# Performance work log

Measured on AMD Instinct MI355X. Metric: run time of the kernel, lower is better.

The kernel has to match this reference:

```python
import jax, jax.numpy as jnp
import numpy as np

EMBED_DIM = 256
NUM_HEADS = 8
HEAD_DIM = EMBED_DIM // NUM_HEADS
SCALE = HEAD_DIM ** -0.5  # note: scale uses head_dim even though attention is over full D
EPS = 1e-12  # torch F.normalize eps


def setup_inputs() -> dict:
    key = jax.random.key(0)
    k1, k2, k3 = jax.random.split(key, 3)
    B, Nq, Nk, D = 4, 4096, 4096, EMBED_DIM
    return {
        "query": jax.random.normal(k1, (B, Nq, D), dtype=jnp.float32),
        "key": jax.random.normal(k2, (B, Nk, D), dtype=jnp.float32),
        "value": jax.random.normal(k3, (B, Nk, D), dtype=jnp.float32),
    }


def _l2_normalize(x):
    # matches torch.nn.functional.normalize(x, dim=-1): x / max(||x||, eps)
    n = jnp.linalg.norm(x, axis=-1, keepdims=True)
    return x / jnp.maximum(n, EPS)


def reference(query, key, value):
    q = _l2_normalize(query)          # (B, Nq, D)
    k = _l2_normalize(key)            # (B, Nk, D)
    scores = jnp.einsum("bqd,bkd->bqk", q, k) * SCALE  # (B, Nq, Nk) cosine sims
    attn = jax.nn.softmax(scores, axis=-1)
    return jnp.einsum("bqk,bkd->bqd", attn, value)     # (B, Nq, D)
```

## Files before the change

### kernel.cpp

```cpp
#include <hip/hip_runtime.h>


#define NQ 4096
#define DIM 256
#define NROWS 16384
#define BM 64
#define BN 64
#define PSTRIDE 68

typedef __attribute__((ext_vector_type(8))) short bf16x8;
typedef __attribute__((ext_vector_type(4))) float f32x4;
typedef __attribute__((ext_vector_type(16))) float f32x16;

__device__ __forceinline__ unsigned short f2bf(float f) {
  unsigned int u = __float_as_uint(f);
  u += 0x7fffu + ((u >> 16) & 1u);
  return (unsigned short)(u >> 16);
}

__device__ __forceinline__ float bf2f(unsigned short h) {
  return __uint_as_float((unsigned int)h << 16);
}

__device__ __forceinline__ unsigned int pack2bf(float a, float b) {
  unsigned int ua = __float_as_uint(a) + 0x8000u;
  unsigned int ub = __float_as_uint(b) + 0x8000u;
  return __builtin_amdgcn_perm(ub, ua, 0x07060302u);
}

__device__ __forceinline__ void gload16(const void* g, void* l) {
  __builtin_amdgcn_global_load_lds(
      (const __attribute__((address_space(1))) unsigned int*)g,
      (__attribute__((address_space(3))) unsigned int*)l, 16, 0, 0);
}

__global__ __launch_bounds__(256) void prep(
    const float* __restrict__ K, const float* __restrict__ V,
    unsigned short* __restrict__ Kfm, unsigned short* __restrict__ Vfm)
{
  __shared__ unsigned short vt[32 * 264];
  const int blk = blockIdx.x, tid = threadIdx.x;
  const int wave = tid >> 6, lane = tid & 63;
  if (blk < 512) {
    const int kt2 = blk;
    const int kt = kt2 >> 1, h = kt2 & 1;
    #pragma unroll
    for (int i = 0; i < 8; i++) {
      const int r = wave*8 + i;
      float4 v = *(const float4*)(K + ((size_t)kt2*32 + r) * DIM + lane * 4);
      float ss = v.x*v.x + v.y*v.y + v.z*v.z + v.w*v.w;
      #pragma unroll
      for (int off = 1; off < 64; off <<= 1) ss += __shfl_xor(ss, off, 64);
      float scale = 1.0f / fmaxf(sqrtf(ss), 1e-12f);
      ushort4 o;
      o.x = f2bf(v.x*scale); o.y = f2bf(v.y*scale);
      o.z = f2bf(v.z*scale); o.w = f2bf(v.w*scale);
      *(ushort4*)(vt + r*264 + lane*4) = o;
    }
    __syncthreads();
    #pragma unroll
    for (int s = 0; s < 4; s++) {
      const int ch = tid + 256*s;
      const int c = ch >> 5, r = ch & 31;
      const int n = h*32 + r;
      bf16x8 val = *(const bf16x8*)(vt + r*264 + c*8);
      *(bf16x8*)(Kfm + (size_t)kt*16384 + (size_t)(c*64 + n)*8) = val;
    }
  } else {
    const int NS = blk - 512;
    #pragma unroll
    for (int i = 0; i < 4; i++) {
      const int e = tid + 256*i;
      const int nl = e >> 6, d = (e & 63) * 4;
      float4 v = *(const float4*)(V + ((size_t)NS*16 + nl)*DIM + d);
      ushort4 o;
      o.x = f2bf(v.x); o.y = f2bf(v.y); o.z = f2bf(v.z); o.w = f2bf(v.w);
      *(ushort4*)(vt + nl*264 + d) = o;
    }
    __syncthreads();
    #pragma unroll
    for (int i = 0; i < 2; i++) {
      const int ch = tid + 256*i;
      const int db = ch >> 6, ln = ch & 63;
      const int row0 = (ln >> 5) * 8, dd = db*32 + (ln & 31);
      ushort4 a, b;
      a.x = vt[(row0+0)*264 + dd]; a.y = vt[(row0+1)*264 + dd];
      a.z = vt[(row0+2)*264 + dd]; a.w = vt[(row0+3)*264 + dd];
      b.x = vt[(row0+4)*264 + dd]; b.y = vt[(row0+5)*264 + dd];
      b.z = vt[(row0+6)*264 + dd]; b.w = vt[(row0+7)*264 + dd];
      size_t base = ((size_t)(NS*8 + db)*64 + ln)*8;
      *(ushort4*)(Vfm + base)     = a;
      *(ushort4*)(Vfm + base + 4) = b;
    }
  }
}

template<int KS>
__global__ __launch_bounds__(256, 3) void attn(
    const float* __restrict__ Qg,
    const unsigned short* __restrict__ Kfm,
    const unsigned short* __restrict__ Vfm,
    unsigned short* __restrict__ Opart, float* __restrict__ lpart)
{
  constexpr int NITER = (NQ / KS) / BN;
  __shared__ unsigned short Klds[32 * 64 * 8];
  __shared__ unsigned short Plds[BM * PSTRIDE];

  const int tid = threadIdx.x, wave = tid >> 6, lane = tid & 63;
  const int l15 = lane & 15, l4 = lane >> 4;
  const int blk = blockIdx.x;
  const int g = blk & (4*KS - 1), qt = blk / (4*KS);
  const int b = g / KS, ks = g & (KS - 1);
  const int Rq0 = b*NQ + qt*BM;
  const int n0base = b*NQ + ks*(NQ/KS);
  const int mi = wave & 1, ni = wave >> 1;

  {
    unsigned short* Qlds = Klds;
    #pragma unroll
    for (int i = 0; i < 16; i++) {
      const int r = wave*16 + i;
      float4 v = *(const float4*)(Qg + (size_t)(Rq0 + r)*DIM + lane*4);
      float ss = v.x*v.x + v.y*v.y + v.z*v.z + v.w*v.w;
      #pragma unroll
      for (int off = 1; off < 64; off <<= 1) ss += __shfl_xor(ss, off, 64);
      float scale = (0.17677669529663687f * 1.4426950408889634f)
                    / fmaxf(sqrtf(ss), 1e-12f);
      ushort4 o;
      o.x = f2bf(v.x*scale); o.y = f2bf(v.y*scale);
      o.z = f2bf(v.z*scale); o.w = f2bf(v.w*scale);
      *(ushort4*)(Qlds + r*DIM + lane*4) = o;
    }
  }
  __syncthreads();

  bf16x8 qf[2][8];
  #pragma unroll
  for (int mt = 0; mt < 2; mt++) {
    const unsigned short* qrow = Klds + (mi*32 + mt*16 + l15)*DIM + l4*8;
    #pragma unroll
    for (int kg = 0; kg < 8; kg++)
      qf[mt][kg] = *(const bf16x8*)(qrow + kg*32);
  }
  __syncthreads();

  f32x16 oacc[2][2] = {};
  float lacc[2] = {};

  auto stage = [&](int kt_) {
    const unsigned short* src = Kfm + (size_t)((n0base + kt_*BN) >> 6) * (32*64*8);
    #pragma unroll
    for (int jj = 0; jj < 4; jj++) {
      const int c = wave*8 + jj*2;
      gload16(src + (size_t)c*512 + lane*8,     Klds + (size_t)c*512);
      gload16(src + (size_t)(c+1)*512 + lane*8, Klds + (size_t)(c+1)*512);
    }
  };

  stage(0);

  for (int kt = 0; kt < NITER; kt++) {
    __syncthreads();

    f32x4 sacc[2][2] = {};
    #pragma unroll
    for (int nt = 0; nt < 2; nt++) {
      const int nrow = ni*32 + nt*16 + l15;
      #pragma unroll
      for (int kg = 0; kg < 8; kg++) {
        const int c = kg*4 + l4;
        bf16x8 kf = *(const bf16x8*)(Klds + ((size_t)(c*64 + nrow))*8);
        __builtin_amdgcn_s_setprio(1);
        #pragma unroll
        for (int mt = 0; mt < 2; mt++)
          sacc[nt][mt] = __builtin_amdgcn_mfma_f32_16x16x32_bf16(
              kf, qf[mt][kg], sacc[nt][mt], 0, 0, 0);
        __builtin_amdgcn_s_setprio(0);
      }
    }

    #pragma unroll
    for (int nt = 0; nt < 2; nt++)
      #pragma unroll
      for (int mt = 0; mt < 2; mt++) {
        float p0 = __builtin_amdgcn_exp2f(sacc[nt][mt][0]);
        float p1 = __builtin_amdgcn_exp2f(sacc[nt][mt][1]);
        float p2 = __builtin_amdgcn_exp2f(sacc[nt][mt][2]);
        float p3 = __builtin_amdgcn_exp2f(sacc[nt][mt][3]);
        lacc[mt] += (p0 + p1) + (p2 + p3);
        uint2 pk;
        pk.x = pack2bf(p0, p1);
        pk.y = pack2bf(p2, p3);
        const int m = mi*32 + mt*16 + l15;
        const int n = ni*32 + nt*16 + 4*l4;
        *(uint2*)(Plds + m*PSTRIDE + n) = pk;
      }

    __syncthreads();

    if (kt + 1 < NITER) stage(kt + 1);

    const int NB0 = (n0base + kt*BN) >> 4;
    #pragma unroll
    for (int kstep = 0; kstep < 4; kstep++) {
      bf16x8 pf[2], vf[2];
      #pragma unroll
      for (int mt2 = 0; mt2 < 2; mt2++)
        pf[mt2] = *(const bf16x8*)(Plds + (mt2*32 + (lane & 31))*PSTRIDE
                                   + kstep*16 + 8*(lane >> 5));
      #pragma unroll
      for (int dt = 0; dt < 2; dt++) {
        const int db = wave*2 + dt;
        vf[dt] = *(const bf16x8*)(Vfm + ((size_t)((NB0 + kstep)*8 + db)*64 + lane)*8);
      }
      __builtin_amdgcn_s_setprio(1);
      #pragma unroll
      for (int mt2 = 0; mt2 < 2; mt2++)
        #pragma unroll
        for (int dt = 0; dt < 2; dt++)
          oacc[mt2][dt] = __builtin_amdgcn_mfma_f32_32x32x16_bf16(
              pf[mt2], vf[dt], oacc[mt2][dt], 0, 0, 0);
      __builtin_amdgcn_s_setprio(0);
    }
  }

  #pragma unroll
  for (int mt = 0; mt < 2; mt++) {
    float s = lacc[mt];
    s += __shfl_xor(s, 16, 64);
    s += __shfl_xor(s, 32, 64);
    if (l4 == 0)
      lpart[(size_t)(ks*2 + ni)*NROWS + Rq0 + mi*32 + mt*16 + l15] = s;
  }

  #pragma unroll
  for (int mt2 = 0; mt2 < 2; mt2++)
    #pragma unroll
    for (int dt = 0; dt < 2; dt++)
      #pragma unroll
      for (int reg = 0; reg < 16; reg++) {
        const int m = mt2*32 + 4*(lane >> 5) + (reg & 3) + 8*(reg >> 2);
        const int d = wave*64 + dt*32 + (lane & 31);
        Opart[((size_t)(ks*NROWS + Rq0 + m))*DIM + d] = f2bf(oacc[mt2][dt][reg]);
      }
}

template<int KS>
__global__ __launch_bounds__(256) void combine(
    const unsigned short* __restrict__ Opart, const float* __restrict__ lpart,
    float* __restrict__ out)
{
  const size_t idx = (size_t)blockIdx.x*256 + threadIdx.x;
  const size_t e = idx*4;
  const int R = (int)(e >> 8);
  float ls = 0.0f;
  #pragma unroll
  for (int i = 0; i < 2*KS; i++) ls += lpart[(size_t)i*NROWS + R];
  float inv = 1.0f / ls;
  float4 o = {0.0f, 0.0f, 0.0f, 0.0f};
  #pragma unroll
  for (int s = 0; s < KS; s++) {
    ushort4 op = *(const ushort4*)(Opart + (size_t)s*NROWS*DIM + e);
    o.x += bf2f(op.x); o.y += bf2f(op.y);
    o.z += bf2f(op.z); o.w += bf2f(op.w);
  }
  o.x *= inv; o.y *= inv; o.z *= inv; o.w *= inv;
  *(float4*)(out + e) = o;
}

extern "C" void kernel_launch(void* const* d_in, const int* in_sizes, int n_in,
                              void* d_out, int out_size, void* d_ws, size_t ws_size,
                              hipStream_t stream) {
  const float* Q = (const float*)d_in[0];
  const float* K = (const float*)d_in[1];
  const float* V = (const float*)d_in[2];
  char* ws = (char*)d_ws;
  unsigned short* Kfm   = (unsigned short*)(ws);
  unsigned short* Vfm   = (unsigned short*)(ws + 8388608);
  unsigned short* Opart = (unsigned short*)(ws + 16777216);

  prep<<<1536, 256, 0, stream>>>(K, V, Kfm, Vfm);

  const size_t need4 = 16777216ull + 4ull*NROWS*DIM*2 + 8ull*NROWS*4;
  if (ws_size >= need4) {
    float* lpart = (float*)(ws + 16777216 + 4ull*NROWS*DIM*2);
    attn<4><<<1024, 256, 0, stream>>>(Q, Kfm, Vfm, Opart, lpart);
    combine<4><<<4096, 256, 0, stream>>>(Opart, lpart, (float*)d_out);
  } else {
    float* lpart = (float*)(ws + 16777216 + 2ull*NROWS*DIM*2);
    attn<2><<<512, 256, 0, stream>>>(Q, Kfm, Vfm, Opart, lpart);
    combine<2><<<4096, 256, 0, stream>>>(Opart, lpart, (float*)d_out);
  }
}
```

Before: 205.6 us.

## Drop key split and combine kernel; use 512-thread blocks over full keys

Removes the split-K partitioning of keys and the separate combine kernel. Each block now has 8 waves and processes a 64-query tile over all 4096 keys, normalizing in-kernel through shared-memory row sums and writing fp32 output directly. This removes the bf16 partial-output round trip and one launch, but the grid shrinks to 256 blocks at one block per CU, which lowers occupancy and latency hiding. Per-wave work also shrinks: a 16-key slice of each tile for scores and a 32-column slice of the output, so V fragments are read from global memory with less reuse per wave.

```diff
diff --git a/kernel.cpp b/kernel.cpp
--- a/kernel.cpp
+++ b/kernel.cpp
@@ -6,6 +6,7 @@
 #define NROWS 16384
 #define BM 64
 #define BN 64
+#define NITER 64
 #define PSTRIDE 68
 
 typedef __attribute__((ext_vector_type(8))) short bf16x8;
@@ -95,31 +96,30 @@
   }
 }
 
-template<int KS>
-__global__ __launch_bounds__(256, 3) void attn(
+__global__ __launch_bounds__(512, 1) void attn(
     const float* __restrict__ Qg,
     const unsigned short* __restrict__ Kfm,
     const unsigned short* __restrict__ Vfm,
-    unsigned short* __restrict__ Opart, float* __restrict__ lpart)
+    float* __restrict__ out)
 {
-  constexpr int NITER = (NQ / KS) / BN;
   __shared__ unsigned short Klds[32 * 64 * 8];
   __shared__ unsigned short Plds[BM * PSTRIDE];
+  __shared__ float Llds[4][BM];
+  __shared__ float Linv[BM];
 
   const int tid = threadIdx.x, wave = tid >> 6, lane = tid & 63;
   const int l15 = lane & 15, l4 = lane >> 4;
   const int blk = blockIdx.x;
-  const int g = blk & (4*KS - 1), qt = blk / (4*KS);
-  const int b = g / KS, ks = g & (KS - 1);
+  const int b = blk & 3, qt = blk >> 2;
   const int Rq0 = b*NQ + qt*BM;
-  const int n0base = b*NQ + ks*(NQ/KS);
+  const int n0base = b*NQ;
   const int mi = wave & 1, ni = wave >> 1;
 
   {
     unsigned short* Qlds = Klds;
     #pragma unroll
-    for (int i = 0; i < 16; i++) {
-      const int r = wave*16 + i;
+    for (int i = 0; i < 8; i++) {
+      const int r = wave*8 + i;
       float4 v = *(const float4*)(Qg + (size_t)(Rq0 + r)*DIM + lane*4);
       float ss = v.x*v.x + v.y*v.y + v.z*v.z + v.w*v.w;
       #pragma unroll
@@ -144,16 +144,15 @@
   }
   __syncthreads();
 
-  f32x16 oacc[2][2] = {};
+  f32x16 oacc[2] = {};
   float lacc[2] = {};
 
   auto stage = [&](int kt_) {
     const unsigned short* src = Kfm + (size_t)((n0base + kt_*BN) >> 6) * (32*64*8);
     #pragma unroll
     for (int jj = 0; jj < 4; jj++) {
-      const int c = wave*8 + jj*2;
-      gload16(src + (size_t)c*512 + lane*8,     Klds + (size_t)c*512);
-      gload16(src + (size_t)(c+1)*512 + lane*8, Klds + (size_t)(c+1)*512);
+      const int c = wave*4 + jj;
+      gload16(src + (size_t)c*512 + lane*8, Klds + (size_t)c*512);
     }
   };
 
@@ -162,39 +161,34 @@
   for (int kt = 0; kt < NITER; kt++) {
     __syncthreads();
 
-    f32x4 sacc[2][2] = {};
-    #pragma unroll
-    for (int nt = 0; nt < 2; nt++) {
-      const int nrow = ni*32 + nt*16 + l15;
-      #pragma unroll
-      for (int kg = 0; kg < 8; kg++) {
-        const int c = kg*4 + l4;
-        bf16x8 kf = *(const bf16x8*)(Klds + ((size_t)(c*64 + nrow))*8);
-        __builtin_amdgcn_s_setprio(1);
-        #pragma unroll
-        for (int mt = 0; mt < 2; mt++)
-          sacc[nt][mt] = __builtin_amdgcn_mfma_f32_16x16x32_bf16(
-              kf, qf[mt][kg], sacc[nt][mt], 0, 0, 0);
-        __builtin_amdgcn_s_setprio(0);
-      }
-    }
-
-    #pragma unroll
-    for (int nt = 0; nt < 2; nt++)
-      #pragma unroll
-      for (int mt = 0; mt < 2; mt++) {
-        float p0 = __builtin_amdgcn_exp2f(sacc[nt][mt][0]);
-        float p1 = __builtin_amdgcn_exp2f(sacc[nt][mt][1]);
-        float p2 = __builtin_amdgcn_exp2f(sacc[nt][mt][2]);
-        float p3 = __builtin_amdgcn_exp2f(sacc[nt][mt][3]);
-        lacc[mt] += (p0 + p1) + (p2 + p3);
-        uint2 pk;
-        pk.x = pack2bf(p0, p1);
-        pk.y = pack2bf(p2, p3);
-        const int m = mi*32 + mt*16 + l15;
-        const int n = ni*32 + nt*16 + 4*l4;
-        *(uint2*)(Plds + m*PSTRIDE + n) = pk;
-      }
+    f32x4 sacc[2] = {};
+    #pragma unroll
+    for (int kg = 0; kg < 8; kg++) {
+      const int nrow = ni*16 + l15;
+      const int c = kg*4 + l4;
+      bf16x8 kf = *(const bf16x8*)(Klds + ((size_t)(c*64 + nrow))*8);
+      __builtin_amdgcn_s_setprio(1);
+      #pragma unroll
+      for (int mt = 0; mt < 2; mt++)
+        sacc[mt] = __builtin_amdgcn_mfma_f32_16x16x32_bf16(
+            kf, qf[mt][kg], sacc[mt], 0, 0, 0);
+      __builtin_amdgcn_s_setprio(0);
+    }
+
+    #pragma unroll
+    for (int mt = 0; mt < 2; mt++) {
+      float p0 = __builtin_amdgcn_exp2f(sacc[mt][0]);
+      float p1 = __builtin_amdgcn_exp2f(sacc[mt][1]);
+      float p2 = __builtin_amdgcn_exp2f(sacc[mt][2]);
+      float p3 = __builtin_amdgcn_exp2f(sacc[mt][3]);
+      lacc[mt] += (p0 + p1) + (p2 + p3);
+      uint2 pk;
+      pk.x = pack2bf(p0, p1);
+      pk.y = pack2bf(p2, p3);
+      const int m = mi*32 + mt*16 + l15;
+      const int n = ni*16 + 4*l4;
+      *(uint2*)(Plds + m*PSTRIDE + n) = pk;
+    }
 
     __syncthreads();
 
@@ -203,23 +197,17 @@
     const int NB0 = (n0base + kt*BN) >> 4;
     #pragma unroll
     for (int kstep = 0; kstep < 4; kstep++) {
-      bf16x8 pf[2], vf[2];
+      bf16x8 pf[2], vf;
       #pragma unroll
       for (int mt2 = 0; mt2 < 2; mt2++)
         pf[mt2] = *(const bf16x8*)(Plds + (mt2*32 + (lane & 31))*PSTRIDE
                                    + kstep*16 + 8*(lane >> 5));
-      #pragma unroll
-      for (int dt = 0; dt < 2; dt++) {
-        const int db = wave*2 + dt;
-        vf[dt] = *(const bf16x8*)(Vfm + ((size_t)((NB0 + kstep)*8 + db)*64 + lane)*8);
-      }
+      vf = *(const bf16x8*)(Vfm + ((size_t)((NB0 + kstep)*8 + wave)*64 + lane)*8);
       __builtin_amdgcn_s_setprio(1);
       #pragma unroll
       for (int mt2 = 0; mt2 < 2; mt2++)
-        #pragma unroll
-        for (int dt = 0; dt < 2; dt++)
-          oacc[mt2][dt] = __builtin_amdgcn_mfma_f32_32x32x16_bf16(
-              pf[mt2], vf[dt], oacc[mt2][dt], 0, 0, 0);
+        oacc[mt2] = __builtin_amdgcn_mfma_f32_32x32x16_bf16(
+            pf[mt2], vf, oacc[mt2], 0, 0, 0);
       __builtin_amdgcn_s_setprio(0);
     }
   }
@@ -230,42 +218,23 @@
     s += __shfl_xor(s, 16, 64);
     s += __shfl_xor(s, 32, 64);
     if (l4 == 0)
-      lpart[(size_t)(ks*2 + ni)*NROWS + Rq0 + mi*32 + mt*16 + l15] = s;
-  }
-
+      Llds[ni][mi*32 + mt*16 + l15] = s;
+  }
+  __syncthreads();
+  if (tid < BM) {
+    float ls = Llds[0][tid] + Llds[1][tid] + Llds[2][tid] + Llds[3][tid];
+    Linv[tid] = 1.0f / ls;
+  }
+  __syncthreads();
+
+  const int d = wave*32 + (lane & 31);
   #pragma unroll
   for (int mt2 = 0; mt2 < 2; mt2++)
     #pragma unroll
-    for (int dt = 0; dt < 2; dt++)
-      #pragma unroll
-      for (int reg = 0; reg < 16; reg++) {
-        const int m = mt2*32 + 4*(lane >> 5) + (reg & 3) + 8*(reg >> 2);
-        const int d = wave*64 + dt*32 + (lane & 31);
-        Opart[((size_t)(ks*NROWS + Rq0 + m))*DIM + d] = f2bf(oacc[mt2][dt][reg]);
-      }
-}
-
-template<int KS>
-__global__ __launch_bounds__(256) void combine(
-    const unsigned short* __restrict__ Opart, const float* __restrict__ lpart,
-    float* __restrict__ out)
-{
-  const size_t idx = (size_t)blockIdx.x*256 + threadIdx.x;
-  const size_t e = idx*4;
-  const int R = (int)(e >> 8);
-  float ls = 0.0f;
-  #pragma unroll
-  for (int i = 0; i < 2*KS; i++) ls += lpart[(size_t)i*NROWS + R];
-  float inv = 1.0f / ls;
-  float4 o = {0.0f, 0.0f, 0.0f, 0.0f};
-  #pragma unroll
-  for (int s = 0; s < KS; s++) {
-    ushort4 op = *(const ushort4*)(Opart + (size_t)s*NROWS*DIM + e);
-    o.x += bf2f(op.x); o.y += bf2f(op.y);
-    o.z += bf2f(op.z); o.w += bf2f(op.w);
-  }
-  o.x *= inv; o.y *= inv; o.z *= inv; o.w *= inv;
-  *(float4*)(out + e) = o;
+    for (int reg = 0; reg < 16; reg++) {
+      const int m = mt2*32 + 4*(lane >> 5) + (reg & 3) + 8*(reg >> 2);
+      out[(size_t)(Rq0 + m)*DIM + d] = oacc[mt2][reg] * Linv[m];
+    }
 }
 
 extern "C" void kernel_launch(void* const* d_in, const int* in_sizes, int n_in,
@@ -275,20 +244,9 @@
   const float* K = (const float*)d_in[1];
   const float* V = (const float*)d_in[2];
   char* ws = (char*)d_ws;
-  unsigned short* Kfm   = (unsigned short*)(ws);
-  unsigned short* Vfm   = (unsigned short*)(ws + 8388608);
-  unsigned short* Opart = (unsigned short*)(ws + 16777216);
+  unsigned short* Kfm = (unsigned short*)(ws);
+  unsigned short* Vfm = (unsigned short*)(ws + 8388608);
 
   prep<<<1536, 256, 0, stream>>>(K, V, Kfm, Vfm);
-
-  const size_t need4 = 16777216ull + 4ull*NROWS*DIM*2 + 8ull*NROWS*4;
-  if (ws_size >= need4) {
-    float* lpart = (float*)(ws + 16777216 + 4ull*NROWS*DIM*2);
-    attn<4><<<1024, 256, 0, stream>>>(Q, Kfm, Vfm, Opart, lpart);
-    combine<4><<<4096, 256, 0, stream>>>(Opart, lpart, (float*)d_out);
-  } else {
-    float* lpart = (float*)(ws + 16777216 + 2ull*NROWS*DIM*2);
-    attn<2><<<512, 256, 0, stream>>>(Q, Kfm, Vfm, Opart, lpart);
-    combine<2><<<4096, 256, 0, stream>>>(Opart, lpart, (float*)d_out);
-  }
-}
+  attn<<<256, 512, 0, stream>>>(Q, Kfm, Vfm, (float*)d_out);
+}
```

Result: slower. 224.2 us (+9.0%).
